# Performance work log

Hardware: AMD Instinct MI355X
Metric: run time of the kernel (lower is better)

The kernel has to match this reference:

```python
import jax, jax.numpy as jnp
import numpy as np

B, T, D = 4, 2048, 768
H = 12
HD = D // H
WINDOW = 128

def setup_inputs() -> dict:
    key = jax.random.key(0)
    k1, k2, k3 = jax.random.split(key, 3)
    x = jax.random.normal(k1, (B, T, D), dtype=jnp.float32)
    Wqkv = jax.random.normal(k2, (D, 3 * D), dtype=jnp.float32) * 0.02
    Wout = jax.random.normal(k3, (D, D), dtype=jnp.float32) * 0.02
    return {"x": x, "Wqkv": Wqkv, "Wout": Wout}

def reference(x, Wqkv, Wout):
    Bx, Tx, Dx = x.shape
    qkv = x @ Wqkv                      # [B,T,3D]
    q, k, v = jnp.split(qkv, 3, axis=-1)
    def heads(t):
        return t.reshape(Bx, Tx, H, HD).transpose(0, 2, 1, 3)  # [B,H,T,hd]
    q, k, v = heads(q), heads(k), heads(v)
    scale = 1.0 / jnp.sqrt(jnp.float32(HD))
    scores = jnp.einsum('bhqd,bhkd->bhqk', q, k) * scale       # [B,H,T,T]
    pos = jnp.arange(Tx)
    dist = pos[None, :] - pos[:, None]                          # j - i
    blocked = (dist > 0) | (dist < -WINDOW)                     # causal band
    scores = jnp.where(blocked[None, None], -jnp.inf, scores)
    attn = jax.nn.softmax(scores, axis=-1)
    out = jnp.einsum('bhqk,bhkd->bhqd', attn, v)                # [B,H,T,hd]
    out = out.transpose(0, 2, 1, 3).reshape(Bx, Tx, Dx)
    return out @ Wout
```

## Files before the change

### kernel.cpp

```cpp
#include <hip/hip_runtime.h>
#include <hip/hip_bf16.h>
#include <stdint.h>

typedef unsigned short u16;
typedef __attribute__((ext_vector_type(8))) short short8;
typedef __attribute__((ext_vector_type(8))) __bf16 bf16x8;
typedef __attribute__((ext_vector_type(4))) float f32x4;

constexpr int Bc  = 4;
constexpr int Tc  = 2048;
constexpr int Dc  = 768;
constexpr int Hc  = 12;
constexpr int WINc = 128;

static __device__ __forceinline__ u16 f2bf(float f) {
  union { float f; uint32_t u; } v; v.f = f;
  uint32_t u = v.u;
  return (u16)((u + 0x7fffu + ((u >> 16) & 1u)) >> 16);
}

static __device__ __forceinline__ f32x4 mfma16x16x32(bf16x8 a, bf16x8 b, f32x4 c) {
  return __builtin_amdgcn_mfma_f32_16x16x32_bf16(a, b, c, 0, 0, 0);
}

#define GLOAD_LDS16(gsrc, ldst)                                                \
  __builtin_amdgcn_global_load_lds(                                            \
      (const __attribute__((address_space(1))) void*)(gsrc),                   \
      (__attribute__((address_space(3))) void*)(ldst), 16, 0, 0)

__global__ __launch_bounds__(256) void cvt_f32_to_bf16(const float* __restrict__ in,
                                                       u16* __restrict__ out) {
  const int i = blockIdx.x * 256 + threadIdx.x;
  const float4 f = ((const float4*)in)[i];
  union { u16 h[4]; uint2 u; } pk;
  pk.h[0] = f2bf(f.x); pk.h[1] = f2bf(f.y); pk.h[2] = f2bf(f.z); pk.h[3] = f2bf(f.w);
  ((uint2*)out)[i] = pk.u;
}

__global__ __launch_bounds__(256) void transpose_cvt(const float* __restrict__ W,
                                                     u16* __restrict__ WT,
                                                     int R, int C) {
  __shared__ float tile[64][65];
  const int t  = threadIdx.x;
  const int c0 = blockIdx.x * 64, r0 = blockIdx.y * 64;
#pragma unroll
  for (int i = 0; i < 16; ++i) {
    const int e = i * 256 + t;
    const int r = e >> 6, c = e & 63;
    tile[r][c] = W[(size_t)(r0 + r) * C + c0 + c];
  }
  __syncthreads();
#pragma unroll
  for (int i = 0; i < 16; ++i) {
    const int e = i * 256 + t;
    const int r = e >> 6, c = e & 63;
    WT[(size_t)(c0 + r) * R + r0 + c] = f2bf(tile[c][r]);
  }
}

template <int EPI>
__global__ __launch_bounds__(256) void gemm_bt(const u16* __restrict__ A,
                                               const u16* __restrict__ Bt,
                                               u16* __restrict__ q_ws,
                                               u16* __restrict__ k_ws,
                                               u16* __restrict__ v_ws,
                                               float* __restrict__ fout) {
  __shared__ u16 As[128][64];
  __shared__ u16 Bs[128][64];
  const int t  = threadIdx.x;
  const int w  = t >> 6, l = t & 63;
  const int lr = l & 15, lh = l >> 4;
  const int wm = w >> 1, wn = w & 1;
  const int m0 = blockIdx.y * 128, n0 = blockIdx.x * 128;

  f32x4 acc[4][4];
#pragma unroll
  for (int mi = 0; mi < 4; ++mi)
#pragma unroll
    for (int ni = 0; ni < 4; ++ni) acc[mi][ni] = f32x4{0.f, 0.f, 0.f, 0.f};

  const int srow = w * 8 + (l >> 3);
  const int scol = ((l & 7) ^ (l >> 3)) * 8;
  const u16* aP = A  + (size_t)(m0 + srow) * 768 + scol;
  const u16* bP = Bt + (size_t)(n0 + srow) * 768 + scol;
  char* asB = (char*)As + w * 1024;
  char* bsB = (char*)Bs + w * 1024;

  for (int kt = 0; kt < 12; ++kt) {
    const int ko = kt * 64;
    __syncthreads();
#pragma unroll
    for (int j = 0; j < 4; ++j) {
      GLOAD_LDS16(aP + ko + j * (32 * 768), asB + j * 4096);
      GLOAD_LDS16(bP + ko + j * (32 * 768), bsB + j * 4096);
    }
    __syncthreads();

#pragma unroll
    for (int kk = 0; kk < 2; ++kk) {
      const int cb = (kk * 64 + lh * 16) ^ ((lr & 7) << 4);
      bf16x8 af[4], bfr[4];
#pragma unroll
      for (int mi = 0; mi < 4; ++mi)
        af[mi] = *(const bf16x8*)((const char*)As + (wm * 64 + mi * 16 + lr) * 128 + cb);
#pragma unroll
      for (int ni = 0; ni < 4; ++ni)
        bfr[ni] = *(const bf16x8*)((const char*)Bs + (wn * 64 + ni * 16 + lr) * 128 + cb);
#pragma unroll
      for (int mi = 0; mi < 4; ++mi)
#pragma unroll
        for (int ni = 0; ni < 4; ++ni)
          acc[mi][ni] = mfma16x16x32(af[mi], bfr[ni], acc[mi][ni]);
    }
  }

  if (EPI == 0) {
#pragma unroll
    for (int mi = 0; mi < 4; ++mi)
#pragma unroll
      for (int ni = 0; ni < 4; ++ni) {
        const int col   = n0 + wn * 64 + ni * 16 + lr;
        const int which = col / 768;
        const int rem   = col - which * 768;
        const int h     = rem >> 6, d = rem & 63;
        u16* dst = (which == 0) ? q_ws : ((which == 1) ? k_ws : v_ws);
        const float scl = (which == 0) ? 0.125f : 1.0f;
#pragma unroll
        for (int r = 0; r < 4; ++r) {
          const int m  = m0 + wm * 64 + mi * 16 + lh * 4 + r;
          const int bb = m >> 11, tt = m & 2047;
          dst[(((size_t)(bb * Hc + h) * Tc + tt) << 6) + d] = f2bf(acc[mi][ni][r] * scl);
        }
      }
  } else {
#pragma unroll
    for (int mi = 0; mi < 4; ++mi)
#pragma unroll
      for (int ni = 0; ni < 4; ++ni) {
        const int col = n0 + wn * 64 + ni * 16 + lr;
#pragma unroll
        for (int r = 0; r < 4; ++r) {
          const int m = m0 + wm * 64 + mi * 16 + lh * 4 + r;
          fout[(size_t)m * 768 + col] = acc[mi][ni][r];
        }
      }
  }
}

__global__ __launch_bounds__(256) void swa_attn(const u16* __restrict__ Q,
                                                const u16* __restrict__ Kk,
                                                const u16* __restrict__ V,
                                                u16* __restrict__ Out) {
  __shared__ u16 Qs[64][72];
  __shared__ u16 Ks[64][72];
  __shared__ u16 Vt[64][72];
  __shared__ u16 Ps[4][16][72];

  const int t  = threadIdx.x;
  const int w  = t >> 6, l = t & 63;
  const int lr = l & 15, lh = l >> 4;
  const int bh = blockIdx.y;
  const int q0 = blockIdx.x * 64;
  const size_t head_base = (size_t)bh * Tc * 64;

  {
    const int row = t >> 2, c = (t & 3) * 16;
    const short8* src = (const short8*)(Q + head_base + (size_t)(q0 + row) * 64 + c);
    *(short8*)&Qs[row][c]     = src[0];
    *(short8*)&Qs[row][c + 8] = src[1];
  }

  float m_r[4], l_r[4];
  f32x4 Oa[4];
#pragma unroll
  for (int r = 0; r < 4; ++r) { m_r[r] = -1e30f; l_r[r] = 0.f; }
#pragma unroll
  for (int n = 0; n < 4; ++n) Oa[n] = f32x4{0.f, 0.f, 0.f, 0.f};

  const int kb_lo = (q0 >= WINc) ? q0 - WINc : 0;
  for (int kb = kb_lo; kb <= q0; kb += 64) {
    __syncthreads();
    {
      const int row = t >> 2, c = (t & 3) * 16;
      const short8* ksrc = (const short8*)(Kk + head_base + (size_t)(kb + row) * 64 + c);
      *(short8*)&Ks[row][c]     = ksrc[0];
      *(short8*)&Ks[row][c + 8] = ksrc[1];
      const short8* vsrc = (const short8*)(V + head_base + (size_t)(kb + row) * 64 + c);
      short8 v0 = vsrc[0], v1 = vsrc[1];
#pragma unroll
      for (int j = 0; j < 8; ++j) {
        Vt[c + j][row]     = (u16)v0[j];
        Vt[c + 8 + j][row] = (u16)v1[j];
      }
    }
    __syncthreads();

    bf16x8 qa0 = *(const bf16x8*)&Qs[w * 16 + lr][lh * 8];
    bf16x8 qa1 = *(const bf16x8*)&Qs[w * 16 + lr][32 + lh * 8];

    f32x4 s[4];
#pragma unroll
    for (int sub = 0; sub < 4; ++sub) {
      bf16x8 kb0 = *(const bf16x8*)&Ks[sub * 16 + lr][lh * 8];
      bf16x8 kb1 = *(const bf16x8*)&Ks[sub * 16 + lr][32 + lh * 8];
      f32x4 z = f32x4{0.f, 0.f, 0.f, 0.f};
      z = mfma16x16x32(qa0, kb0, z);
      z = mfma16x16x32(qa1, kb1, z);
      s[sub] = z;
    }

    const int qbase = q0 + w * 16 + lh * 4;
#pragma unroll
    for (int sub = 0; sub < 4; ++sub) {
      const int kj = kb + sub * 16 + lr;
#pragma unroll
      for (int r = 0; r < 4; ++r) {
        const int qi = qbase + r;
        const bool ok = (kj <= qi) && (kj + WINc >= qi);
        s[sub][r] = ok ? s[sub][r] : -1e30f;
      }
    }

    float mt[4];
#pragma unroll
    for (int r = 0; r < 4; ++r)
      mt[r] = fmaxf(fmaxf(s[0][r], s[1][r]), fmaxf(s[2][r], s[3][r]));
#pragma unroll
    for (int msk = 1; msk < 16; msk <<= 1)
#pragma unroll
      for (int r = 0; r < 4; ++r)
        mt[r] = fmaxf(mt[r], __shfl_xor(mt[r], msk, 64));

    float al[4];
#pragma unroll
    for (int r = 0; r < 4; ++r) {
      const float mn = fmaxf(m_r[r], mt[r]);
      al[r] = __expf(m_r[r] - mn);
      m_r[r] = mn;
    }

    float rs[4] = {0.f, 0.f, 0.f, 0.f};
#pragma unroll
    for (int sub = 0; sub < 4; ++sub)
#pragma unroll
      for (int r = 0; r < 4; ++r) {
        const float p = __expf(s[sub][r] - m_r[r]);
        s[sub][r] = p;
        rs[r] += p;
      }
#pragma unroll
    for (int msk = 1; msk < 16; msk <<= 1)
#pragma unroll
      for (int r = 0; r < 4; ++r)
        rs[r] += __shfl_xor(rs[r], msk, 64);
#pragma unroll
    for (int r = 0; r < 4; ++r) l_r[r] = l_r[r] * al[r] + rs[r];

#pragma unroll
    for (int n = 0; n < 4; ++n)
#pragma unroll
      for (int r = 0; r < 4; ++r) Oa[n][r] *= al[r];

#pragma unroll
    for (int sub = 0; sub < 4; ++sub)
#pragma unroll
      for (int r = 0; r < 4; ++r)
        Ps[w][lh * 4 + r][sub * 16 + lr] = f2bf(s[sub][r]);

#pragma unroll
    for (int ks = 0; ks < 2; ++ks) {
      bf16x8 pa = *(const bf16x8*)&Ps[w][lr][ks * 32 + lh * 8];
#pragma unroll
      for (int n = 0; n < 4; ++n) {
        bf16x8 vb = *(const bf16x8*)&Vt[n * 16 + lr][ks * 32 + lh * 8];
        Oa[n] = mfma16x16x32(pa, vb, Oa[n]);
      }
    }
  }

  const int bb = bh / Hc, h = bh - bb * Hc;
#pragma unroll
  for (int n = 0; n < 4; ++n)
#pragma unroll
    for (int r = 0; r < 4; ++r) {
      const float val = Oa[n][r] / l_r[r];
      const int ti = q0 + w * 16 + lh * 4 + r;
      Out[((size_t)(bb * Tc + ti)) * 768 + h * 64 + n * 16 + lr] = f2bf(val);
    }
}

extern "C" void kernel_launch(void* const* d_in, const int* in_sizes, int n_in,
                              void* d_out, int out_size, void* d_ws, size_t ws_size,
                              hipStream_t stream) {
  (void)in_sizes; (void)n_in; (void)out_size; (void)ws_size;
  const float* x    = (const float*)d_in[0];
  const float* Wqkv = (const float*)d_in[1];
  const float* Wout = (const float*)d_in[2];
  float* out = (float*)d_out;

  u16* ws    = (u16*)d_ws;
  u16* xb    = ws;
  u16* wqkvT = xb + 6291456;
  u16* woutT = wqkvT + 1769472;
  u16* qws   = woutT + 589824;
  u16* kws   = qws + 6291456;
  u16* vws   = kws + 6291456;
  u16* aws   = xb;

  cvt_f32_to_bf16<<<6144, 256, 0, stream>>>(x, xb);
  transpose_cvt<<<dim3(36, 12), 256, 0, stream>>>(Wqkv, wqkvT, 768, 2304);
  transpose_cvt<<<dim3(12, 12), 256, 0, stream>>>(Wout, woutT, 768, 768);
  gemm_bt<0><<<dim3(18, 64), 256, 0, stream>>>(xb, wqkvT, qws, kws, vws, nullptr);
  swa_attn<<<dim3(32, 48), 256, 0, stream>>>(qws, kws, vws, aws);
  gemm_bt<1><<<dim3(6, 64), 256, 0, stream>>>(aws, woutT, nullptr, nullptr, nullptr, out);
}
```

Measured before the change: 110.7 us.

## Merge prep kernels and preload all attention K/V tiles up front

Three preprocessing launches (x conversion and two weight transposes) become a single prep kernel that branches on block index, saving two launches. The attention kernel now issues global loads for all (up to three) K/V tiles before storing them to LDS and synchronizing once. This removes the per-tile barrier pairs and lets the loads overlap. Q fragments are read straight from global memory into registers. The cost is more LDS (three K and three V buffers) and registers, which may lower occupancy.

```diff
diff --git a/kernel.cpp b/kernel.cpp
--- a/kernel.cpp
+++ b/kernel.cpp
@@ -28,21 +28,28 @@
       (const __attribute__((address_space(1))) void*)(gsrc),                   \
       (__attribute__((address_space(3))) void*)(ldst), 16, 0, 0)
 
-__global__ __launch_bounds__(256) void cvt_f32_to_bf16(const float* __restrict__ in,
-                                                       u16* __restrict__ out) {
-  const int i = blockIdx.x * 256 + threadIdx.x;
-  const float4 f = ((const float4*)in)[i];
-  union { u16 h[4]; uint2 u; } pk;
-  pk.h[0] = f2bf(f.x); pk.h[1] = f2bf(f.y); pk.h[2] = f2bf(f.z); pk.h[3] = f2bf(f.w);
-  ((uint2*)out)[i] = pk.u;
-}
-
-__global__ __launch_bounds__(256) void transpose_cvt(const float* __restrict__ W,
-                                                     u16* __restrict__ WT,
-                                                     int R, int C) {
+__global__ __launch_bounds__(256) void prep(const float* __restrict__ x,
+                                            u16* __restrict__ xb,
+                                            const float* __restrict__ Wqkv,
+                                            u16* __restrict__ wqkvT,
+                                            const float* __restrict__ Wout,
+                                            u16* __restrict__ woutT) {
   __shared__ float tile[64][65];
-  const int t  = threadIdx.x;
-  const int c0 = blockIdx.x * 64, r0 = blockIdx.y * 64;
+  const int t = threadIdx.x;
+  const int b = blockIdx.x;
+  if (b < 6144) {
+    const int i = b * 256 + t;
+    const float4 f = ((const float4*)x)[i];
+    union { u16 h[4]; uint2 u; } pk;
+    pk.h[0] = f2bf(f.x); pk.h[1] = f2bf(f.y); pk.h[2] = f2bf(f.z); pk.h[3] = f2bf(f.w);
+    ((uint2*)xb)[i] = pk.u;
+    return;
+  }
+  const float* W; u16* WT; int C, bx, by;
+  if (b < 6576) { W = Wqkv; WT = wqkvT; C = 2304; const int bb = b - 6144; bx = bb % 36; by = bb / 36; }
+  else          { W = Wout; WT = woutT; C = 768;  const int bb = b - 6576; bx = bb % 12; by = bb / 12; }
+  const int R = 768;
+  const int c0 = bx * 64, r0 = by * 64;
 #pragma unroll
   for (int i = 0; i < 16; ++i) {
     const int e = i * 256 + t;
@@ -151,9 +158,8 @@
                                                 const u16* __restrict__ Kk,
                                                 const u16* __restrict__ V,
                                                 u16* __restrict__ Out) {
-  __shared__ u16 Qs[64][72];
-  __shared__ u16 Ks[64][72];
-  __shared__ u16 Vt[64][72];
+  __shared__ u16 Ks[3][64][72];
+  __shared__ u16 Vt[3][64][72];
   __shared__ u16 Ps[4][16][72];
 
   const int t  = threadIdx.x;
@@ -163,12 +169,38 @@
   const int q0 = blockIdx.x * 64;
   const size_t head_base = (size_t)bh * Tc * 64;
 
-  {
-    const int row = t >> 2, c = (t & 3) * 16;
-    const short8* src = (const short8*)(Q + head_base + (size_t)(q0 + row) * 64 + c);
-    *(short8*)&Qs[row][c]     = src[0];
-    *(short8*)&Qs[row][c + 8] = src[1];
-  }
+  const int kb_lo = (q0 >= WINc) ? q0 - WINc : 0;
+  const int nt    = ((q0 - kb_lo) >> 6) + 1;
+
+  const u16* qrow = Q + head_base + (size_t)(q0 + w * 16 + lr) * 64;
+  const bf16x8 qa0 = *(const bf16x8*)(qrow + lh * 8);
+  const bf16x8 qa1 = *(const bf16x8*)(qrow + 32 + lh * 8);
+
+  const int row = t >> 2, c = (t & 3) * 16;
+  short8 kreg[3][2], vreg[3][2];
+#pragma unroll
+  for (int ti = 0; ti < 3; ++ti) {
+    if (ti < nt) {
+      const int kb = kb_lo + ti * 64;
+      const short8* ksrc = (const short8*)(Kk + head_base + (size_t)(kb + row) * 64 + c);
+      const short8* vsrc = (const short8*)(V  + head_base + (size_t)(kb + row) * 64 + c);
+      kreg[ti][0] = ksrc[0]; kreg[ti][1] = ksrc[1];
+      vreg[ti][0] = vsrc[0]; vreg[ti][1] = vsrc[1];
+    }
+  }
+#pragma unroll
+  for (int ti = 0; ti < 3; ++ti) {
+    if (ti < nt) {
+      *(short8*)&Ks[ti][row][c]     = kreg[ti][0];
+      *(short8*)&Ks[ti][row][c + 8] = kreg[ti][1];
+#pragma unroll
+      for (int j = 0; j < 8; ++j) {
+        Vt[ti][c + j][row]     = (u16)vreg[ti][0][j];
+        Vt[ti][c + 8 + j][row] = (u16)vreg[ti][1][j];
+      }
+    }
+  }
+  __syncthreads();
 
   float m_r[4], l_r[4];
   f32x4 Oa[4];
@@ -177,32 +209,16 @@
 #pragma unroll
   for (int n = 0; n < 4; ++n) Oa[n] = f32x4{0.f, 0.f, 0.f, 0.f};
 
-  const int kb_lo = (q0 >= WINc) ? q0 - WINc : 0;
-  for (int kb = kb_lo; kb <= q0; kb += 64) {
-    __syncthreads();
-    {
-      const int row = t >> 2, c = (t & 3) * 16;
-      const short8* ksrc = (const short8*)(Kk + head_base + (size_t)(kb + row) * 64 + c);
-      *(short8*)&Ks[row][c]     = ksrc[0];
-      *(short8*)&Ks[row][c + 8] = ksrc[1];
-      const short8* vsrc = (const short8*)(V + head_base + (size_t)(kb + row) * 64 + c);
-      short8 v0 = vsrc[0], v1 = vsrc[1];
-#pragma unroll
-      for (int j = 0; j < 8; ++j) {
-        Vt[c + j][row]     = (u16)v0[j];
-        Vt[c + 8 + j][row] = (u16)v1[j];
-      }
-    }
-    __syncthreads();
-
-    bf16x8 qa0 = *(const bf16x8*)&Qs[w * 16 + lr][lh * 8];
-    bf16x8 qa1 = *(const bf16x8*)&Qs[w * 16 + lr][32 + lh * 8];
+#pragma unroll
+  for (int ti = 0; ti < 3; ++ti) {
+    if (ti >= nt) break;
+    const int kb = kb_lo + ti * 64;
 
     f32x4 s[4];
 #pragma unroll
     for (int sub = 0; sub < 4; ++sub) {
-      bf16x8 kb0 = *(const bf16x8*)&Ks[sub * 16 + lr][lh * 8];
-      bf16x8 kb1 = *(const bf16x8*)&Ks[sub * 16 + lr][32 + lh * 8];
+      const bf16x8 kb0 = *(const bf16x8*)&Ks[ti][sub * 16 + lr][lh * 8];
+      const bf16x8 kb1 = *(const bf16x8*)&Ks[ti][sub * 16 + lr][32 + lh * 8];
       f32x4 z = f32x4{0.f, 0.f, 0.f, 0.f};
       z = mfma16x16x32(qa0, kb0, z);
       z = mfma16x16x32(qa1, kb1, z);
@@ -269,10 +285,10 @@
 
 #pragma unroll
     for (int ks = 0; ks < 2; ++ks) {
-      bf16x8 pa = *(const bf16x8*)&Ps[w][lr][ks * 32 + lh * 8];
+      const bf16x8 pa = *(const bf16x8*)&Ps[w][lr][ks * 32 + lh * 8];
 #pragma unroll
       for (int n = 0; n < 4; ++n) {
-        bf16x8 vb = *(const bf16x8*)&Vt[n * 16 + lr][ks * 32 + lh * 8];
+        const bf16x8 vb = *(const bf16x8*)&Vt[ti][n * 16 + lr][ks * 32 + lh * 8];
         Oa[n] = mfma16x16x32(pa, vb, Oa[n]);
       }
     }
@@ -280,13 +296,14 @@
 
   const int bb = bh / Hc, h = bh - bb * Hc;
 #pragma unroll
-  for (int n = 0; n < 4; ++n)
-#pragma unroll
-    for (int r = 0; r < 4; ++r) {
-      const float val = Oa[n][r] / l_r[r];
-      const int ti = q0 + w * 16 + lh * 4 + r;
-      Out[((size_t)(bb * Tc + ti)) * 768 + h * 64 + n * 16 + lr] = f2bf(val);
-    }
+  for (int r = 0; r < 4; ++r) {
+    const float inv = 1.f / l_r[r];
+    const int ti = q0 + w * 16 + lh * 4 + r;
+#pragma unroll
+    for (int n = 0; n < 4; ++n)
+      Out[((size_t)(bb * Tc + ti)) * 768 + h * 64 + n * 16 + lr] =
+          f2bf(Oa[n][r] * inv);
+  }
 }
 
 extern "C" void kernel_launch(void* const* d_in, const int* in_sizes, int n_in,
@@ -307,9 +324,7 @@
   u16* vws   = kws + 6291456;
   u16* aws   = xb;
 
-  cvt_f32_to_bf16<<<6144, 256, 0, stream>>>(x, xb);
-  transpose_cvt<<<dim3(36, 12), 256, 0, stream>>>(Wqkv, wqkvT, 768, 2304);
-  transpose_cvt<<<dim3(12, 12), 256, 0, stream>>>(Wout, woutT, 768, 768);
+  prep<<<6720, 256, 0, stream>>>(x, xb, Wqkv, wqkvT, Wout, woutT);
   gemm_bt<0><<<dim3(18, 64), 256, 0, stream>>>(xb, wqkvT, qws, kws, vws, nullptr);
   swa_attn<<<dim3(32, 48), 256, 0, stream>>>(qws, kws, vws, aws);
   gemm_bt<1><<<dim3(6, 64), 256, 0, stream>>>(aws, woutT, nullptr, nullptr, nullptr, out);
```

Measured after the change: 107.7 us. -2.8%, faster.
